# Kernel optimization log

Measured on AMD Instinct MI355X. Metric: run time of the kernel, lower is better.

The kernel has to match this reference:

```python
import jax, jax.numpy as jnp
import numpy as np

N, IN_F, H, D = 4096, 256, 4, 64  # nodes, in_features, num_heads, head_dim
NEG_BIG = -9e15


def setup_inputs() -> dict:
    key = jax.random.key(0)
    k1, k2, k3, k4, k5 = jax.random.split(key, 5)
    x = jax.random.normal(k1, (N, IN_F), dtype=jnp.float32)
    adj = jax.random.randint(k2, (N, N), 0, 2, dtype=jnp.int32)
    # xavier-uniform-scale init for W: [in_features, H*D]
    lim_w = float(np.sqrt(6.0 / (IN_F + H * D)))
    W = jax.random.uniform(k3, (IN_F, H * D), minval=-lim_w, maxval=lim_w, dtype=jnp.float32)
    # a: [2*D, 1] split into a1 (dest half) and a2 (source half)
    lim_a = float(np.sqrt(6.0 / (2 * D + 1)))
    a1 = jax.random.uniform(k4, (D,), minval=-lim_a, maxval=lim_a, dtype=jnp.float32)
    a2 = jax.random.uniform(k5, (D,), minval=-lim_a, maxval=lim_a, dtype=jnp.float32)
    return {"x": x, "adj": adj, "W": W, "a1": a1, "a2": a2}


def reference(x, adj, W, a1, a2):
    n = x.shape[0]
    h = (x @ W).reshape(n, H, D)                      # [N, H, D]
    # e[i,j,h] = leaky_relu(<h_i, a1> + <h_j, a2>)  (== concat([h_i,h_j]) @ a)
    si = jnp.einsum("nhd,d->nh", h, a1)               # [N, H]
    sj = jnp.einsum("nhd,d->nh", h, a2)               # [N, H]
    e = jax.nn.leaky_relu(si[:, None, :] + sj[None, :, :], negative_slope=0.2)
    e = jnp.where(adj[:, :, None] > 0, e, NEG_BIG)    # mask non-edges
    att = jax.nn.softmax(e, axis=1)                   # softmax over neighbors j
    out = jnp.einsum("ijh,jhd->ihd", att, h)          # per-head aggregation
    return out.reshape(n, H * D)                      # concat heads
```

## Files before the change

kernel.cpp:

```cpp
#include <hip/hip_runtime.h>
#include <hip/hip_bf16.h>


typedef __bf16 bf16x8 __attribute__((ext_vector_type(8)));
typedef float floatx4 __attribute__((ext_vector_type(4)));

#define LOG2E 1.4426950408889634f
#define NN 4096

__device__ __forceinline__ void gl16(const void* g, void* l) {
  __builtin_amdgcn_global_load_lds(
      (const __attribute__((address_space(1))) unsigned int*)g,
      (__attribute__((address_space(3))) unsigned int*)l, 16, 0, 0);
}

__global__ __launch_bounds__(256) void gat_pack(const int* __restrict__ adj,
                                                unsigned char* __restrict__ adjb) {
  int T = blockIdx.x * 256 + threadIdx.x;
  const int stride = 2048 * 256;
#pragma unroll
  for (int it = 0; it < 4; ++it, T += stride) {
    const int* p = adj + (size_t)T * 8;
    int4 a = *(const int4*)p;
    int4 b = *(const int4*)(p + 4);
    unsigned int m = 0;
    m |= (a.x != 0) ? 1u : 0u;
    m |= (a.y != 0) ? 2u : 0u;
    m |= (a.z != 0) ? 4u : 0u;
    m |= (a.w != 0) ? 8u : 0u;
    m |= (b.x != 0) ? 16u : 0u;
    m |= (b.y != 0) ? 32u : 0u;
    m |= (b.z != 0) ? 64u : 0u;
    m |= (b.w != 0) ? 128u : 0u;
    adjb[T] = (unsigned char)m;
  }
}

__global__ __launch_bounds__(256) void gat_prep(
    const float* __restrict__ x, const float* __restrict__ W,
    const float* __restrict__ a1, const float* __restrict__ a2,
    __bf16* __restrict__ hT, float* __restrict__ siT, float2* __restrict__ vv2T,
    float* __restrict__ sjm) {
  __shared__ float hl[32 * 68];
  __shared__ float sjb[32];
  const int t = threadIdx.x;
  const int it = blockIdx.x, hh = blockIdx.y;
  const int i0 = it * 32, c0 = hh * 64;
  const int tr = t >> 4, tc = t & 15;

  float acc[2][4] = {{0.f,0.f,0.f,0.f},{0.f,0.f,0.f,0.f}};
  const float* xr = x + (size_t)(i0 + tr * 2) * 256;
  const float* wp = W + c0 + tc * 4;
  for (int k = 0; k < 256; k += 4) {
    float4 xv0 = *(const float4*)(xr + k);
    float4 xv1 = *(const float4*)(xr + 256 + k);
    float xs[2][4] = {{xv0.x, xv0.y, xv0.z, xv0.w},
                      {xv1.x, xv1.y, xv1.z, xv1.w}};
#pragma unroll
    for (int kk = 0; kk < 4; ++kk) {
      float4 wv = *(const float4*)(wp + (size_t)(k + kk) * 256);
#pragma unroll
      for (int i = 0; i < 2; ++i) {
        acc[i][0] = fmaf(xs[i][kk], wv.x, acc[i][0]);
        acc[i][1] = fmaf(xs[i][kk], wv.y, acc[i][1]);
        acc[i][2] = fmaf(xs[i][kk], wv.z, acc[i][2]);
        acc[i][3] = fmaf(xs[i][kk], wv.w, acc[i][3]);
      }
    }
  }

  float4 a1v = *(const float4*)(a1 + tc * 4);
  float4 a2v = *(const float4*)(a2 + tc * 4);
#pragma unroll
  for (int i = 0; i < 2; ++i) {
    float s1 = acc[i][0]*a1v.x + acc[i][1]*a1v.y + acc[i][2]*a1v.z + acc[i][3]*a1v.w;
    float s2 = acc[i][0]*a2v.x + acc[i][1]*a2v.y + acc[i][2]*a2v.z + acc[i][3]*a2v.w;
#pragma unroll
    for (int off = 1; off < 16; off <<= 1) {
      s1 += __shfl_xor(s1, off);
      s2 += __shfl_xor(s2, off);
    }
    if (tc == 0) {
      int r = tr * 2 + i;
      siT[hh * NN + i0 + r] = s1 * LOG2E;
      float sjs = s2 * LOG2E;
      vv2T[hh * NN + i0 + r] =
          make_float2(__builtin_amdgcn_exp2f(sjs), __builtin_amdgcn_exp2f(0.2f * sjs));
      sjb[r] = sjs;
    }
    *(float4*)&hl[(tr * 2 + i) * 68 + tc * 4] =
        make_float4(acc[i][0], acc[i][1], acc[i][2], acc[i][3]);
  }
  __syncthreads();

  if (t < 32) {
    float v = sjb[t];
#pragma unroll
    for (int off = 1; off < 32; off <<= 1) v = fmaxf(v, __shfl_xor(v, off));
    if (t == 0) sjm[it * 4 + hh] = v;
  }

  const int d = t & 63, g = t >> 6;
  bf16x8 h0;
#pragma unroll
  for (int ii = 0; ii < 8; ++ii) h0[ii] = (__bf16)hl[(g * 8 + ii) * 68 + d];
  *(bf16x8*)(hT + (size_t)(hh * 64 + d) * NN + i0 + g * 8) = h0;
}

__global__ __launch_bounds__(256, 2) void gat_attn(
    const __bf16* __restrict__ hT, const float* __restrict__ siT,
    const float2* __restrict__ vv2T, const float* __restrict__ sjm,
    const unsigned char* __restrict__ adjb, float* __restrict__ out) {
  __shared__ __align__(16) char lds[51200];
  const int t = threadIdx.x;
  const int w = t >> 6, lane = t & 63, quad = lane >> 4, l16 = lane & 15;
  const int i0 = blockIdx.x * 32, hh = blockIdx.y;

  const __bf16* hTw = hT + (size_t)hh * 64 * NN;
  const float2* vw = vv2T + hh * NN;

#pragma unroll
  for (int k = 0; k < 4; ++k) {
    int s = (w * 4 + k) * 64 + lane;
    int r = s >> 5, slot = s & 31, c = slot ^ r;
    gl16(adjb + (size_t)(i0 + r) * 512 + c * 16, lds + 34816 + s * 16);
  }

  int hoff[4];
#pragma unroll
  for (int nt = 0; nt < 4; ++nt)
    hoff[nt] = (nt * 16 + l16) * NN + w * 32 + quad * 8;

#pragma unroll
  for (int nt = 0; nt < 4; ++nt)
    gl16(hTw + hoff[nt], lds + ((w * 4 + nt) << 10) + (lane << 4));
  if (w == 0)
    gl16(vw + (quad * 32 + l16 * 2), lds + 32768 + (lane << 4));

  float vv = fmaxf(sjm[lane * 4 + hh], sjm[(lane + 64) * 4 + hh]);
#pragma unroll
  for (int off = 1; off < 64; off <<= 1) vv = fmaxf(vv, __shfl_xor(vv, off));
  float u[2], u2[2];
#pragma unroll
  for (int mt = 0; mt < 2; ++mt) {
    float sis = siT[hh * NN + i0 + mt * 16 + l16];
    float tt = sis + vv;
    float m = fmaxf(tt, 0.2f * tt);
    u[mt] = __builtin_amdgcn_exp2f(sis - m);
    u2[mt] = __builtin_amdgcn_exp2f(0.2f * sis - m);
  }

  bf16x8 ones;
#pragma unroll
  for (int ii = 0; ii < 8; ++ii) ones[ii] = (__bf16)1.0f;

  floatx4 zv = {0.f, 0.f, 0.f, 0.f};
  floatx4 acc[2][4], lacc[2];
#pragma unroll
  for (int mt = 0; mt < 2; ++mt) {
    lacc[mt] = zv;
#pragma unroll
    for (int nt = 0; nt < 4; ++nt) acc[mt][nt] = zv;
  }

  __syncthreads();

  for (int win = 0; win < 32; ++win) {
    const int p = win & 1;
    const char* hb = lds + (p << 14);
    const char* vb = lds + 32768 + (p << 10);

    if (win + 1 < 32) {
      const int jn = (win + 1) << 7;
      char* hbn = lds + ((p ^ 1) << 14);
#pragma unroll
      for (int nt = 0; nt < 4; ++nt)
        gl16(hTw + hoff[nt] + jn, hbn + ((w * 4 + nt) << 10) + (lane << 4));
      if (w == 0)
        gl16(vw + jn + quad * 32 + l16 * 2,
             lds + 32768 + ((p ^ 1) << 10) + (lane << 4));
    }

    unsigned int m0 = *(const unsigned int*)(lds + 34816 + (l16 << 9) +
                                             ((win ^ l16) << 4) + (w << 2));
    unsigned int m1 = *(const unsigned int*)(lds + 34816 + ((16 + l16) << 9) +
                                             ((win ^ (16 + l16)) << 4) + (w << 2));
    bf16x8 bfr[4];
#pragma unroll
    for (int nt = 0; nt < 4; ++nt)
      bfr[nt] = *(const bf16x8*)(hb + ((w * 4 + nt) << 10) + (lane << 4));
    float4 q[4];
#pragma unroll
    for (int c = 0; c < 4; ++c)
      q[c] = *(const float4*)(vb + (w << 8) + (quad << 6) + (c << 4));

#pragma unroll
    for (int mt = 0; mt < 2; ++mt) {
      unsigned int m8 = ((mt ? m1 : m0) >> (quad * 8)) & 0xffu;
      bf16x8 af;
#pragma unroll
      for (int c = 0; c < 4; ++c) {
        float p0 = fmaxf(u[mt] * q[c].x, u2[mt] * q[c].y);
        float p1 = fmaxf(u[mt] * q[c].z, u2[mt] * q[c].w);
        af[2 * c]     = ((m8 >> (2 * c)) & 1u)     ? (__bf16)p0 : (__bf16)0.f;
        af[2 * c + 1] = ((m8 >> (2 * c + 1)) & 1u) ? (__bf16)p1 : (__bf16)0.f;
      }
#pragma unroll
      for (int nt = 0; nt < 4; ++nt)
        acc[mt][nt] = __builtin_amdgcn_mfma_f32_16x16x32_bf16(af, bfr[nt],
                                                              acc[mt][nt], 0, 0, 0);
      lacc[mt] = __builtin_amdgcn_mfma_f32_16x16x32_bf16(af, ones, lacc[mt], 0, 0, 0);
    }
    __syncthreads();
  }

  float* accs = (float*)lds;
  float* lsum = (float*)(lds + 34816);
#pragma unroll
  for (int mt = 0; mt < 2; ++mt)
#pragma unroll
    for (int reg = 0; reg < 4; ++reg) {
      int row = mt * 16 + quad * 4 + reg;
      float* ap = accs + (w * 32 + row) * 68;
#pragma unroll
      for (int nt = 0; nt < 4; ++nt)
        ap[nt * 16 + l16] = acc[mt][nt][reg];
      if (l16 == 0) lsum[w * 32 + row] = lacc[mt][reg];
    }
  __syncthreads();

  const int r = t >> 3, c = (t & 7) * 8;
  float l = lsum[r] + lsum[32 + r] + lsum[64 + r] + lsum[96 + r];
  float inv = 1.0f / l;
  float o[8];
#pragma unroll
  for (int k = 0; k < 8; ++k)
    o[k] = (accs[r * 68 + c + k] + accs[(32 + r) * 68 + c + k] +
            accs[(64 + r) * 68 + c + k] + accs[(96 + r) * 68 + c + k]) * inv;
  float* op = out + (size_t)(i0 + r) * 256 + hh * 64 + c;
  *(float4*)op = make_float4(o[0], o[1], o[2], o[3]);
  *(float4*)(op + 4) = make_float4(o[4], o[5], o[6], o[7]);
}

extern "C" void kernel_launch(void* const* d_in, const int* in_sizes, int n_in,
                              void* d_out, int out_size, void* d_ws, size_t ws_size,
                              hipStream_t stream) {
  const float* x  = (const float*)d_in[0];
  const int*   adj = (const int*)d_in[1];
  const float* W  = (const float*)d_in[2];
  const float* a1 = (const float*)d_in[3];
  const float* a2 = (const float*)d_in[4];
  float* out = (float*)d_out;
  char* ws = (char*)d_ws;

  __bf16* hT   = (__bf16*)ws;
  float*  siT  = (float*)(ws + 2097152);
  float2* vv2T = (float2*)(ws + 2162688);
  float*  sjm  = (float*)(ws + 2293760);
  unsigned char* adjb = (unsigned char*)(ws + 2295808);

  gat_pack<<<2048, 256, 0, stream>>>(adj, adjb);
  gat_prep<<<dim3(128, 4), 256, 0, stream>>>(x, W, a1, a2, hT, siT, vv2T, sjm);
  gat_attn<<<dim3(128, 4), 256, 0, stream>>>(hT, siT, vv2T, sjm, adjb, out);
}
```

Baseline: 165.0 us.

## Split attention over source halves with 64-row tiles and separate reduce kernel

```diff
diff --git a/kernel.cpp b/kernel.cpp
--- a/kernel.cpp
+++ b/kernel.cpp
@@ -110,39 +110,40 @@
 __global__ __launch_bounds__(256, 2) void gat_attn(
     const __bf16* __restrict__ hT, const float* __restrict__ siT,
     const float2* __restrict__ vv2T, const float* __restrict__ sjm,
-    const unsigned char* __restrict__ adjb, float* __restrict__ out) {
-  __shared__ __align__(16) char lds[51200];
+    const unsigned int* __restrict__ adjw,
+    float* __restrict__ pacc, float* __restrict__ pl) {
+  __shared__ __align__(16) char lds[35328];
   const int t = threadIdx.x;
   const int w = t >> 6, lane = t & 63, quad = lane >> 4, l16 = lane & 15;
-  const int i0 = blockIdx.x * 32, hh = blockIdx.y;
-
-  const __bf16* hTw = hT + (size_t)hh * 64 * NN;
-  const float2* vw = vv2T + hh * NN;
-
-#pragma unroll
-  for (int k = 0; k < 4; ++k) {
-    int s = (w * 4 + k) * 64 + lane;
-    int r = s >> 5, slot = s & 31, c = slot ^ r;
-    gl16(adjb + (size_t)(i0 + r) * 512 + c * 16, lds + 34816 + s * 16);
-  }
+  const int i0 = blockIdx.x * 64, hh = blockIdx.y, s = blockIdx.z;
+  const int jbeg = s * 2048;
+
+  const __bf16* hTw = hT + (size_t)hh * 64 * NN + jbeg + w * 32 + quad * 8;
+  const float2* vw = vv2T + hh * NN + jbeg;
 
   int hoff[4];
 #pragma unroll
-  for (int nt = 0; nt < 4; ++nt)
-    hoff[nt] = (nt * 16 + l16) * NN + w * 32 + quad * 8;
+  for (int nt = 0; nt < 4; ++nt) hoff[nt] = (nt * 16 + l16) * NN;
+
+  const unsigned int* mp[4];
+#pragma unroll
+  for (int mt = 0; mt < 4; ++mt)
+    mp[mt] = adjw + (size_t)(i0 + mt * 16 + l16) * 128 + (jbeg >> 5) + w;
 
 #pragma unroll
   for (int nt = 0; nt < 4; ++nt)
     gl16(hTw + hoff[nt], lds + ((w * 4 + nt) << 10) + (lane << 4));
-  if (w == 0)
-    gl16(vw + (quad * 32 + l16 * 2), lds + 32768 + (lane << 4));
+  if (w == 0) gl16(vw + lane * 2, lds + 32768 + (lane << 4));
+  unsigned int mc[4], mn[4];
+#pragma unroll
+  for (int mt = 0; mt < 4; ++mt) mc[mt] = mp[mt][0];
 
   float vv = fmaxf(sjm[lane * 4 + hh], sjm[(lane + 64) * 4 + hh]);
 #pragma unroll
   for (int off = 1; off < 64; off <<= 1) vv = fmaxf(vv, __shfl_xor(vv, off));
-  float u[2], u2[2];
-#pragma unroll
-  for (int mt = 0; mt < 2; ++mt) {
+  float u[4], u2[4];
+#pragma unroll
+  for (int mt = 0; mt < 4; ++mt) {
     float sis = siT[hh * NN + i0 + mt * 16 + l16];
     float tt = sis + vv;
     float m = fmaxf(tt, 0.2f * tt);
@@ -155,9 +156,9 @@
   for (int ii = 0; ii < 8; ++ii) ones[ii] = (__bf16)1.0f;
 
   floatx4 zv = {0.f, 0.f, 0.f, 0.f};
-  floatx4 acc[2][4], lacc[2];
-#pragma unroll
-  for (int mt = 0; mt < 2; ++mt) {
+  floatx4 acc[4][4], lacc[4];
+#pragma unroll
+  for (int mt = 0; mt < 4; ++mt) {
     lacc[mt] = zv;
 #pragma unroll
     for (int nt = 0; nt < 4; ++nt) acc[mt][nt] = zv;
@@ -165,26 +166,23 @@
 
   __syncthreads();
 
-  for (int win = 0; win < 32; ++win) {
+  for (int win = 0; win < 16; ++win) {
     const int p = win & 1;
     const char* hb = lds + (p << 14);
     const char* vb = lds + 32768 + (p << 10);
 
-    if (win + 1 < 32) {
+    if (win + 1 < 16) {
+#pragma unroll
+      for (int mt = 0; mt < 4; ++mt) mn[mt] = mp[mt][(win + 1) * 4];
       const int jn = (win + 1) << 7;
       char* hbn = lds + ((p ^ 1) << 14);
 #pragma unroll
       for (int nt = 0; nt < 4; ++nt)
         gl16(hTw + hoff[nt] + jn, hbn + ((w * 4 + nt) << 10) + (lane << 4));
       if (w == 0)
-        gl16(vw + jn + quad * 32 + l16 * 2,
-             lds + 32768 + ((p ^ 1) << 10) + (lane << 4));
-    }
-
-    unsigned int m0 = *(const unsigned int*)(lds + 34816 + (l16 << 9) +
-                                             ((win ^ l16) << 4) + (w << 2));
-    unsigned int m1 = *(const unsigned int*)(lds + 34816 + ((16 + l16) << 9) +
-                                             ((win ^ (16 + l16)) << 4) + (w << 2));
+        gl16(vw + jn + lane * 2, lds + 32768 + ((p ^ 1) << 10) + (lane << 4));
+    }
+
     bf16x8 bfr[4];
 #pragma unroll
     for (int nt = 0; nt < 4; ++nt)
@@ -195,15 +193,17 @@
       q[c] = *(const float4*)(vb + (w << 8) + (quad << 6) + (c << 4));
 
 #pragma unroll
-    for (int mt = 0; mt < 2; ++mt) {
-      unsigned int m8 = ((mt ? m1 : m0) >> (quad * 8)) & 0xffu;
+    for (int mt = 0; mt < 4; ++mt) {
+      unsigned int m8 = mc[mt] >> (quad * 8);
       bf16x8 af;
 #pragma unroll
       for (int c = 0; c < 4; ++c) {
         float p0 = fmaxf(u[mt] * q[c].x, u2[mt] * q[c].y);
         float p1 = fmaxf(u[mt] * q[c].z, u2[mt] * q[c].w);
-        af[2 * c]     = ((m8 >> (2 * c)) & 1u)     ? (__bf16)p0 : (__bf16)0.f;
-        af[2 * c + 1] = ((m8 >> (2 * c + 1)) & 1u) ? (__bf16)p1 : (__bf16)0.f;
+        int b0 = ((int)(m8 << (31 - 2 * c))) >> 31;
+        int b1 = ((int)(m8 << (30 - 2 * c))) >> 31;
+        af[2 * c]     = (__bf16)__uint_as_float(__float_as_uint(p0) & (unsigned)b0);
+        af[2 * c + 1] = (__bf16)__uint_as_float(__float_as_uint(p1) & (unsigned)b1);
       }
 #pragma unroll
       for (int nt = 0; nt < 4; ++nt)
@@ -211,35 +211,72 @@
                                                               acc[mt][nt], 0, 0, 0);
       lacc[mt] = __builtin_amdgcn_mfma_f32_16x16x32_bf16(af, ones, lacc[mt], 0, 0, 0);
     }
+#pragma unroll
+    for (int mt = 0; mt < 4; ++mt) mc[mt] = mn[mt];
     __syncthreads();
   }
 
   float* accs = (float*)lds;
   float* lsum = (float*)(lds + 34816);
-#pragma unroll
-  for (int mt = 0; mt < 2; ++mt)
-#pragma unroll
-    for (int reg = 0; reg < 4; ++reg) {
-      int row = mt * 16 + quad * 4 + reg;
-      float* ap = accs + (w * 32 + row) * 68;
-#pragma unroll
-      for (int nt = 0; nt < 4; ++nt)
-        ap[nt * 16 + l16] = acc[mt][nt][reg];
-      if (l16 == 0) lsum[w * 32 + row] = lacc[mt][reg];
-    }
+  if (w < 2) {
+#pragma unroll
+    for (int mt = 0; mt < 4; ++mt)
+#pragma unroll
+      for (int reg = 0; reg < 4; ++reg) {
+        int row = mt * 16 + quad * 4 + reg;
+        float* ap = accs + (w * 64 + row) * 68;
+#pragma unroll
+        for (int nt = 0; nt < 4; ++nt)
+          ap[nt * 16 + l16] = acc[mt][nt][reg];
+        if (l16 == 0) lsum[w * 64 + row] = lacc[mt][reg];
+      }
+  }
   __syncthreads();
-
-  const int r = t >> 3, c = (t & 7) * 8;
-  float l = lsum[r] + lsum[32 + r] + lsum[64 + r] + lsum[96 + r];
+  if (w >= 2) {
+    const int b = w - 2;
+#pragma unroll
+    for (int mt = 0; mt < 4; ++mt)
+#pragma unroll
+      for (int reg = 0; reg < 4; ++reg) {
+        int row = mt * 16 + quad * 4 + reg;
+        float* ap = accs + (b * 64 + row) * 68;
+#pragma unroll
+        for (int nt = 0; nt < 4; ++nt)
+          ap[nt * 16 + l16] += acc[mt][nt][reg];
+        if (l16 == 0) lsum[b * 64 + row] += lacc[mt][reg];
+      }
+  }
+  __syncthreads();
+
+  const int r = t >> 2, cb = (t & 3) * 16;
+  float* op = pacc + (size_t)s * NN * 256 + (size_t)(i0 + r) * 256 + hh * 64 + cb;
+#pragma unroll
+  for (int c4 = 0; c4 < 4; ++c4) {
+    int c = cb + c4 * 4;
+    float4 o;
+    o.x = accs[r * 68 + c + 0] + accs[(64 + r) * 68 + c + 0];
+    o.y = accs[r * 68 + c + 1] + accs[(64 + r) * 68 + c + 1];
+    o.z = accs[r * 68 + c + 2] + accs[(64 + r) * 68 + c + 2];
+    o.w = accs[r * 68 + c + 3] + accs[(64 + r) * 68 + c + 3];
+    *(float4*)(op + c4 * 4) = o;
+  }
+  if (t < 64)
+    pl[(size_t)s * NN * 4 + (i0 + t) * 4 + hh] = lsum[t] + lsum[64 + t];
+}
+
+__global__ __launch_bounds__(256) void gat_reduce(
+    const float* __restrict__ pacc, const float* __restrict__ pl,
+    float* __restrict__ out) {
+  const int e4 = blockIdx.x * 256 + threadIdx.x;
+  const int e = e4 * 4;
+  const int i = e >> 8;
+  const int h = (e & 255) >> 6;
+  float4 a0 = *(const float4*)(pacc + e);
+  float4 a1 = *(const float4*)(pacc + (size_t)NN * 256 + e);
+  float l = pl[i * 4 + h] + pl[(size_t)NN * 4 + i * 4 + h];
   float inv = 1.0f / l;
-  float o[8];
-#pragma unroll
-  for (int k = 0; k < 8; ++k)
-    o[k] = (accs[r * 68 + c + k] + accs[(32 + r) * 68 + c + k] +
-            accs[(64 + r) * 68 + c + k] + accs[(96 + r) * 68 + c + k]) * inv;
-  float* op = out + (size_t)(i0 + r) * 256 + hh * 64 + c;
-  *(float4*)op = make_float4(o[0], o[1], o[2], o[3]);
-  *(float4*)(op + 4) = make_float4(o[4], o[5], o[6], o[7]);
+  *(float4*)(out + e) = make_float4((a0.x + a1.x) * inv, (a0.y + a1.y) * inv,
+                                    (a0.z + a1.z) * inv, (a0.w + a1.w) * inv);
 }
 
 extern "C" void kernel_launch(void* const* d_in, const int* in_sizes, int n_in,
@@ -258,8 +295,12 @@
   float2* vv2T = (float2*)(ws + 2162688);
   float*  sjm  = (float*)(ws + 2293760);
   unsigned char* adjb = (unsigned char*)(ws + 2295808);
+  float*  pacc = (float*)(ws + 4392960);
+  float*  pl   = (float*)(ws + 12781568);
 
   gat_pack<<<2048, 256, 0, stream>>>(adj, adjb);
   gat_prep<<<dim3(128, 4), 256, 0, stream>>>(x, W, a1, a2, hT, siT, vv2T, sjm);
-  gat_attn<<<dim3(128, 4), 256, 0, stream>>>(hT, siT, vv2T, sjm, adjb, out);
-}
+  gat_attn<<<dim3(64, 4, 2), 256, 0, stream>>>(hT, siT, vv2T, sjm,
+                                               (const unsigned int*)adjb, pacc, pl);
+  gat_reduce<<<1024, 256, 0, stream>>>(pacc, pl, out);
+}
```

Result: no change. 165.1 us (+0.0%).
